# Kernel tuning notes

Measured on AMD Instinct MI355X. Metric: run time of the kernel, lower is better.

The kernel has to match this reference:

```python
import jax, jax.numpy as jnp
import numpy as np

B, N, D_VIS, D_LBL = 64, 256, 2048, 512
H, F_OUT = 8, 256            # n_heads, gat_out_per_head_dim
D_IN = D_VIS + D_LBL         # 2560, GAT input dim
D_GAT = H * F_OUT            # 2048, concat-heads output dim
D_EMB = 512                  # final_embedding_dim
ALPHA = 0.2                  # LeakyReLU negative slope


def setup_inputs() -> dict:
    key = jax.random.key(0)
    ks = jax.random.split(key, 9)
    visual_features = jax.random.normal(ks[0], (B, D_VIS), jnp.float32)
    labels_features = jax.random.normal(ks[1], (N, D_LBL), jnp.float32)
    adj = (jax.random.uniform(ks[2], (N, N)) < 0.1).astype(jnp.float32)
    label_adj_matrix = jnp.maximum(adj, jnp.eye(N, dtype=jnp.float32))
    s = 1.0 / np.sqrt(D_IN)
    W_gat = jax.random.uniform(ks[3], (D_IN, H, F_OUT), jnp.float32, -s, s)
    a_src = jax.random.uniform(ks[4], (H, F_OUT), jnp.float32, -s, s)
    a_dst = jax.random.uniform(ks[5], (H, F_OUT), jnp.float32, -s, s)
    sg = 1.0 / np.sqrt(D_GAT)
    pool_q = jax.random.uniform(ks[6], (D_GAT,), jnp.float32, -sg, sg)
    fc_W = jax.random.uniform(ks[7], (D_GAT, D_EMB), jnp.float32, -sg, sg)
    fc_b = jax.random.uniform(ks[8], (D_EMB,), jnp.float32, -sg, sg)
    return {"visual_features": visual_features, "labels_features": labels_features,
            "label_adj_matrix": label_adj_matrix, "W_gat": W_gat, "a_src": a_src,
            "a_dst": a_dst, "pool_q": pool_q, "fc_W": fc_W, "fc_b": fc_b}


def reference(visual_features, labels_features, label_adj_matrix,
              W_gat, a_src, a_dst, pool_q, fc_W, fc_b):
    # Build per-sample contextualized label node features: (B, N, D_IN)
    x = jnp.concatenate(
        [jnp.broadcast_to(labels_features[None], (B, N, D_LBL)),
         jnp.broadcast_to(visual_features[:, None, :], (B, N, D_VIS))], axis=-1)
    # Multi-head GAT layer, batched over B (the torch code loops over B)
    Wh = jnp.einsum('bnd,dhf->bnhf', x, W_gat)            # (B, N, H, F)
    src = jnp.einsum('bnhf,hf->bhn', Wh, a_src)           # (B, H, N)
    dst = jnp.einsum('bnhf,hf->bhn', Wh, a_dst)           # (B, H, N)
    e = src[:, :, :, None] + dst[:, :, None, :]           # (B, H, N, N)
    e = jnp.where(e > 0, e, ALPHA * e)                    # LeakyReLU
    mask = (label_adj_matrix > 0)[None, None]             # (1, 1, N, N)
    scores = jnp.where(mask, e, jnp.float32(-9e15))
    attn = jax.nn.softmax(scores, axis=-1)                # (B, H, N, N)
    out = jnp.einsum('bhij,bjhf->bihf', attn, Wh)         # (B, N, H, F)
    out = jax.nn.elu(out.reshape(B, N, D_GAT))            # concat heads + ELU
    # attention pooling over label nodes
    pw = jax.nn.softmax(jnp.einsum('bnd,d->bn', out, pool_q), axis=-1)
    pooled = jnp.einsum('bn,bnd->bd', pw, out)            # (B, D_GAT)
    return pooled @ fc_W + fc_b                           # (B, D_EMB)
```

## Files before the change

kernel.cpp:

```cpp
#include <hip/hip_runtime.h>
#include <hip/hip_bf16.h>
#include <math.h>

#define BB 64
#define NN 256
#define D_VIS 2048
#define D_LBL 512
#define HH 8
#define FF 256
#define DG 2048
#define DE 512
#define ALPHA 0.2f
#define PSTRIDE 264

using bf16 = __hip_bfloat16;
using short8 = __attribute__((ext_vector_type(8))) short;
using f32x4  = __attribute__((ext_vector_type(4))) float;
__device__ __forceinline__ float b2f(bf16 x) { return __bfloat162float(x); }
__device__ __forceinline__ unsigned short f2bs(float x) {
    bf16 h = __float2bfloat16(x);
    unsigned short u;
    __builtin_memcpy(&u, &h, 2);
    return u;
}

__global__ void __launch_bounds__(256) k_wh(const float* __restrict__ labels,
                                            const float* __restrict__ visual,
                                            const float* __restrict__ Wg,
                                            unsigned short* __restrict__ WhLbT,
                                            float* __restrict__ WhVz,
                                            const float* __restrict__ aSrc,
                                            const float* __restrict__ aDst,
                                            float* __restrict__ srcLp,
                                            float* __restrict__ dstLp,
                                            float* __restrict__ srcVp,
                                            float* __restrict__ dstVp) {
    __shared__ unsigned short As[32][72];
    __shared__ unsigned short Bs[64][72];
    const int t = threadIdx.x;
    const int w = t >> 6;
    const int lane = t & 63;
    const int l15 = lane & 15, quad = lane >> 4;
    const int n0 = blockIdx.x * 64;
    const int p2 = blockIdx.x & 3;
    const int y = blockIdx.y;
    const bool isL = (y < 8);
    const int q = y - 8;
    const int m0  = isL ? y * 32 : (q & 1) * 32;
    const int z   = isL ? 0 : (q >> 1);
    const int kb0 = z * 512;
    const float* A = isL ? labels : visual;
    const int lda  = isL ? D_LBL : D_VIS;
    const float* Wb = Wg + (isL ? 0 : (size_t)D_LBL * DG);

    f32x4 acc[2];
    acc[0] = (f32x4){0.f, 0.f, 0.f, 0.f};
    acc[1] = (f32x4){0.f, 0.f, 0.f, 0.f};

    for (int kc = 0; kc < 8; ++kc) {
        const int kb = kb0 + kc * 64;
#pragma unroll
        for (int p = 0; p < 2; ++p) {
            const int idx = t + 256 * p;
            const int r = idx >> 4, q4 = idx & 15;
            const float4 v = *(const float4*)(A + (size_t)(m0 + r) * lda + kb + 4 * q4);
            unsigned short s4[4] = {f2bs(v.x), f2bs(v.y), f2bs(v.z), f2bs(v.w)};
            __builtin_memcpy(&As[r][4 * q4], s4, 8);
        }
#pragma unroll
        for (int p = 0; p < 4; ++p) {
            const int kk = (t >> 4) + 16 * p;
            const int c4 = (t & 15) * 4;
            const float4 v = *(const float4*)(Wb + (size_t)(kb + kk) * DG + n0 + c4);
            Bs[c4 + 0][kk] = f2bs(v.x);
            Bs[c4 + 1][kk] = f2bs(v.y);
            Bs[c4 + 2][kk] = f2bs(v.z);
            Bs[c4 + 3][kk] = f2bs(v.w);
        }
        __syncthreads();
#pragma unroll
        for (int ks = 0; ks < 2; ++ks) {
            const short8 bf = *(const short8*)&Bs[w * 16 + l15][ks * 32 + quad * 8];
#pragma unroll
            for (int mi = 0; mi < 2; ++mi) {
                const short8 af = *(const short8*)&As[mi * 16 + l15][ks * 32 + quad * 8];
                acc[mi] = __builtin_amdgcn_mfma_f32_16x16x32_bf16(af, bf, acc[mi], 0, 0, 0);
            }
        }
        __syncthreads();
    }
    const int col = n0 + w * 16 + l15;
    const int h = col >> 8;
    const float as = aSrc[col], ad = aDst[col];
    if (isL) {
#pragma unroll
        for (int mi = 0; mi < 2; ++mi) {
            unsigned short s4[4];
#pragma unroll
            for (int r = 0; r < 4; ++r) s4[r] = f2bs(acc[mi][r]);
            __builtin_memcpy(&WhLbT[(size_t)col * NN + m0 + mi * 16 + quad * 4], s4, 8);
        }
#pragma unroll
        for (int mi = 0; mi < 2; ++mi)
#pragma unroll
            for (int r = 0; r < 4; ++r) {
                float sv = acc[mi][r] * as;
                float dv = acc[mi][r] * ad;
#pragma unroll
                for (int off = 1; off < 16; off <<= 1) {
                    sv += __shfl_xor(sv, off);
                    dv += __shfl_xor(dv, off);
                }
                if (l15 == 0) {
                    const int row = m0 + mi * 16 + quad * 4 + r;
                    srcLp[(p2 * NN + row) * HH + h] = sv;
                    dstLp[(p2 * NN + row) * HH + h] = dv;
                }
            }
    } else {
        float* Wv = WhVz + (size_t)z * BB * DG;
#pragma unroll
        for (int mi = 0; mi < 2; ++mi)
#pragma unroll
            for (int r = 0; r < 4; ++r)
                Wv[(size_t)(m0 + mi * 16 + quad * 4 + r) * DG + col] = acc[mi][r];
        const int pv = p2 * 4 + z;
#pragma unroll
        for (int mi = 0; mi < 2; ++mi)
#pragma unroll
            for (int r = 0; r < 4; ++r) {
                float sv = acc[mi][r] * as;
                float dv = acc[mi][r] * ad;
#pragma unroll
                for (int off = 1; off < 16; off <<= 1) {
                    sv += __shfl_xor(sv, off);
                    dv += __shfl_xor(dv, off);
                }
                if (l15 == 0) {
                    const int row = m0 + mi * 16 + quad * 4 + r;
                    srcVp[(pv * BB + row) * HH + h] = sv;
                    dstVp[(pv * BB + row) * HH + h] = dv;
                }
            }
    }
}

__global__ void __launch_bounds__(512, 4) k_gat(const unsigned short* __restrict__ WhLbT,
                                                const float* __restrict__ WhVz,
                                                const float* __restrict__ srcLp,
                                                const float* __restrict__ dstLp,
                                                const float* __restrict__ srcVp,
                                                const float* __restrict__ dstVp,
                                                const float* __restrict__ adj,
                                                const float* __restrict__ pool_q,
                                                bf16* __restrict__ outb,
                                                float* __restrict__ ps_p) {
    const int bid = blockIdx.x;
    const int it = bid & 3;
    const int h  = (bid >> 2) & 7;
    const int b  = bid >> 5;
    const int i0 = it * 64;
    const int t = threadIdx.x;
    const int w = t >> 6;
    const int lane = t & 63;
    const int l15 = lane & 15, quad = lane >> 4;

    __shared__ __align__(16) unsigned short Pl[64][PSTRIDE];
    __shared__ __align__(16) float dls2[2 * NN];
    __shared__ float slsA[64], slsC[64], slsTE[64], inv[64];
    __shared__ float psl[8][64];

    if (t < NN) {
        float dl = 0.f;
#pragma unroll
        for (int p = 0; p < 4; ++p) dl += dstLp[(p * NN + t) * HH + h];
        dls2[2 * t]     = __expf(dl);
        dls2[2 * t + 1] = __expf(ALPHA * dl);
    }
    if (t < 64) {
        float c = 0.f;
#pragma unroll
        for (int p = 0; p < 16; ++p)
            c += srcVp[(p * BB + b) * HH + h] + dstVp[(p * BB + b) * HH + h];
        float sl = 0.f;
#pragma unroll
        for (int p = 0; p < 4; ++p) sl += srcLp[(p * NN + i0 + t) * HH + h];
        const float u = c + sl;
        slsA[t]  = __expf(u);
        slsC[t]  = __expf(ALPHA * u);
        slsTE[t] = __expf(-u);
    }
    const int n0 = w * 32;
    float wv[2] = {0.f, 0.f};
#pragma unroll
    for (int z = 0; z < 4; ++z)
#pragma unroll
        for (int ni = 0; ni < 2; ++ni)
            wv[ni] += WhVz[(size_t)z * BB * DG + (size_t)b * DG + h * FF + n0 + ni * 16 + l15];
    __syncthreads();

    {
        const int g = lane >> 4, s = lane & 15;
#pragma unroll
        for (int rr = 0; rr < 2; ++rr) {
            const int iloc = w * 8 + rr * 4 + g;
            const int i = i0 + iloc;
            const float Ai = slsA[iloc], Ci = slsC[iloc], TEi = slsTE[iloc];
            float pr[16];
            float sum = 0.f;
#pragma unroll
            for (int jj = 0; jj < 8; ++jj) {
                const int j0 = 2 * s + 32 * jj;
                const float2 av = *(const float2*)(adj + (size_t)i * NN + j0);
                const float4 bd = *(const float4*)&dls2[2 * j0];
                const bool g0 = bd.x > TEi;
                const bool g1 = bd.z > TEi;
                float p0 = (g0 ? Ai : Ci) * (g0 ? bd.x : bd.y);
                float p1 = (g1 ? Ai : Ci) * (g1 ? bd.z : bd.w);
                p0 = av.x > 0.f ? p0 : 0.f;
                p1 = av.y > 0.f ? p1 : 0.f;
                pr[2 * jj] = p0; pr[2 * jj + 1] = p1;
                sum += p0 + p1;
            }
#pragma unroll
            for (int off = 1; off < 16; off <<= 1) sum += __shfl_xor(sum, off);
            if (s == 0) inv[iloc] = 1.0f / sum;
#pragma unroll
            for (int jj = 0; jj < 8; ++jj) {
                const unsigned int pk =
                    ((unsigned int)f2bs(pr[2 * jj + 1]) << 16) | f2bs(pr[2 * jj]);
                *(unsigned int*)&Pl[iloc][2 * s + 32 * jj] = pk;
            }
        }
    }
    __syncthreads();

    f32x4 acc[4][2];
#pragma unroll
    for (int mi = 0; mi < 4; ++mi)
#pragma unroll
        for (int ni = 0; ni < 2; ++ni) acc[mi][ni] = (f32x4){0.f, 0.f, 0.f, 0.f};

    const unsigned short* wb = WhLbT + (size_t)(h * FF + n0 + l15) * NN + quad * 8;
    short8 bc0 = *(const short8*)(wb);
    short8 bc1 = *(const short8*)(wb + (size_t)16 * NN);
#pragma unroll
    for (int kc = 0; kc < 8; ++kc) {
        short8 bn0, bn1;
        if (kc < 7) {
            bn0 = *(const short8*)(wb + (kc + 1) * 32);
            bn1 = *(const short8*)(wb + (size_t)16 * NN + (kc + 1) * 32);
        }
        short8 a[4];
#pragma unroll
        for (int mi = 0; mi < 4; ++mi)
            a[mi] = *(const short8*)&Pl[mi * 16 + l15][kc * 32 + quad * 8];
#pragma unroll
        for (int mi = 0; mi < 4; ++mi)
            acc[mi][0] = __builtin_amdgcn_mfma_f32_16x16x32_bf16(a[mi], bc0, acc[mi][0], 0, 0, 0);
#pragma unroll
        for (int mi = 0; mi < 4; ++mi)
            acc[mi][1] = __builtin_amdgcn_mfma_f32_16x16x32_bf16(a[mi], bc1, acc[mi][1], 0, 0, 0);
        bc0 = bn0; bc1 = bn1;
    }

    const float pqv0 = pool_q[h * FF + n0 + l15];
    const float pqv1 = pool_q[h * FF + n0 + 16 + l15];
#pragma unroll
    for (int mi = 0; mi < 4; ++mi)
#pragma unroll
        for (int r = 0; r < 4; ++r) {
            const int row = mi * 16 + quad * 4 + r;
            const float ivr = inv[row];
            bf16* orow = outb + ((size_t)(b * NN + i0 + row)) * DG + h * FF + n0;
            float x0 = fmaf(acc[mi][0][r], ivr, wv[0]);
            float x1 = fmaf(acc[mi][1][r], ivr, wv[1]);
            x0 = x0 > 0.f ? x0 : (__expf(x0) - 1.0f);
            x1 = x1 > 0.f ? x1 : (__expf(x1) - 1.0f);
            orow[l15]      = __float2bfloat16(x0);
            orow[16 + l15] = __float2bfloat16(x1);
            float dot = fmaf(x0, pqv0, x1 * pqv1);
#pragma unroll
            for (int off = 1; off < 16; off <<= 1) dot += __shfl_xor(dot, off);
            if (l15 == 0) psl[w][row] = dot;
        }
    __syncthreads();
    if (t < 64) {
        float s = 0.f;
#pragma unroll
        for (int ww = 0; ww < 8; ++ww) s += psl[ww][t];
        ps_p[((size_t)h * BB + b) * NN + i0 + t] = s;
    }
}

__global__ void __launch_bounds__(256) k_pool(const bf16* __restrict__ outb,
                                              const float* __restrict__ ps_p,
                                              float* __restrict__ pooled,
                                              const float* __restrict__ fcb,
                                              float* __restrict__ out) {
    const int dt = blockIdx.x;
    const int b  = blockIdx.y;
    const int t  = threadIdx.x;
    if (dt < 2) out[b * DE + dt * 256 + t] = fcb[dt * 256 + t];
    __shared__ float wsm[NN];
    __shared__ float redm[4];
    __shared__ float reds[4];
    float v = 0.f;
#pragma unroll
    for (int s = 0; s < 8; ++s)
        v += ps_p[((size_t)s * BB + b) * NN + t];
    float m = v;
#pragma unroll
    for (int off = 32; off; off >>= 1) m = fmaxf(m, __shfl_xor(m, off));
    if ((t & 63) == 0) redm[t >> 6] = m;
    __syncthreads();
    m = fmaxf(fmaxf(redm[0], redm[1]), fmaxf(redm[2], redm[3]));
    const float e = __expf(v - m);
    float s = e;
#pragma unroll
    for (int off = 32; off; off >>= 1) s += __shfl_xor(s, off);
    if ((t & 63) == 0) reds[t >> 6] = s;
    __syncthreads();
    s = reds[0] + reds[1] + reds[2] + reds[3];
    wsm[t] = e / s;
    __syncthreads();
    const int d = dt * 256 + t;
    float acc = 0.f;
    const bf16* base = outb + (size_t)b * NN * DG + d;
#pragma unroll 8
    for (int n = 0; n < NN; ++n)
        acc = fmaf(wsm[n], b2f(base[(size_t)n * DG]), acc);
    pooled[(size_t)b * DG + d] = acc;
}

__global__ void __launch_bounds__(256) k_mgemm(const float* __restrict__ A, int lda,
                                               const float* __restrict__ W, int ldw,
                                               float* __restrict__ C, int ldc,
                                               int kSlice, int kIters) {
    __shared__ unsigned short As[32][72];
    __shared__ unsigned short Bs[64][72];
    const int t = threadIdx.x;
    const int w = t >> 6;
    const int lane = t & 63;
    const int l15 = lane & 15, quad = lane >> 4;
    const int n0 = blockIdx.x * 64;
    const int m0 = blockIdx.y * 32;
    const int kb0 = blockIdx.z * kSlice;
    f32x4 acc[2];
    acc[0] = (f32x4){0.f, 0.f, 0.f, 0.f};
    acc[1] = (f32x4){0.f, 0.f, 0.f, 0.f};
    for (int kc = 0; kc < kIters; ++kc) {
        const int kb = kb0 + kc * 64;
#pragma unroll
        for (int p = 0; p < 2; ++p) {
            const int idx = t + 256 * p;
            const int r = idx >> 4, q4 = idx & 15;
            const float4 v = *(const float4*)(A + (size_t)(m0 + r) * lda + kb + 4 * q4);
            unsigned short s4[4] = {f2bs(v.x), f2bs(v.y), f2bs(v.z), f2bs(v.w)};
            __builtin_memcpy(&As[r][4 * q4], s4, 8);
        }
#pragma unroll
        for (int p = 0; p < 4; ++p) {
            const int kk = (t >> 4) + 16 * p;
            const int c4 = (t & 15) * 4;
            const float4 v = *(const float4*)(W + (size_t)(kb + kk) * ldw + n0 + c4);
            Bs[c4 + 0][kk] = f2bs(v.x);
            Bs[c4 + 1][kk] = f2bs(v.y);
            Bs[c4 + 2][kk] = f2bs(v.z);
            Bs[c4 + 3][kk] = f2bs(v.w);
        }
        __syncthreads();
#pragma unroll
        for (int ks = 0; ks < 2; ++ks) {
            const short8 bf = *(const short8*)&Bs[w * 16 + l15][ks * 32 + quad * 8];
#pragma unroll
            for (int mi = 0; mi < 2; ++mi) {
                const short8 af = *(const short8*)&As[mi * 16 + l15][ks * 32 + quad * 8];
                acc[mi] = __builtin_amdgcn_mfma_f32_16x16x32_bf16(af, bf, acc[mi], 0, 0, 0);
            }
        }
        __syncthreads();
    }
    const int col = n0 + w * 16 + l15;
#pragma unroll
    for (int mi = 0; mi < 2; ++mi)
#pragma unroll
        for (int r = 0; r < 4; ++r)
            atomicAdd(&C[(size_t)(m0 + mi * 16 + quad * 4 + r) * ldc + col], acc[mi][r]);
}

extern "C" void kernel_launch(void* const* d_in, const int* in_sizes, int n_in,
                              void* d_out, int out_size, void* d_ws, size_t ws_size,
                              hipStream_t stream) {
    (void)in_sizes; (void)n_in; (void)out_size; (void)ws_size;
    const float* visual = (const float*)d_in[0];
    const float* labels = (const float*)d_in[1];
    const float* adj    = (const float*)d_in[2];
    const float* Wg     = (const float*)d_in[3];
    const float* a_src  = (const float*)d_in[4];
    const float* a_dst  = (const float*)d_in[5];
    const float* pool_q = (const float*)d_in[6];
    const float* fcW    = (const float*)d_in[7];
    const float* fcb    = (const float*)d_in[8];
    float* out = (float*)d_out;

    float* ws_f   = (float*)d_ws;
    float* WhVz   = ws_f;
    float* srcLp  = WhVz + 4 * BB * DG;
    float* dstLp  = srcLp + 4 * NN * HH;
    float* srcVp  = dstLp + 4 * NN * HH;
    float* dstVp  = srcVp + 16 * BB * HH;
    float* ps_p   = dstVp + 16 * BB * HH;
    float* pooled = ps_p + 8 * BB * NN;
    bf16*  outb   = (bf16*)(pooled + BB * DG);
    unsigned short* WhLbT = (unsigned short*)(outb + (size_t)BB * NN * DG);

    k_wh<<<dim3(DG / 64, 16), 256, 0, stream>>>(labels, visual, Wg, WhLbT, WhVz,
                                                a_src, a_dst, srcLp, dstLp, srcVp, dstVp);

    k_gat<<<BB * HH * 4, 512, 0, stream>>>(WhLbT, WhVz, srcLp, dstLp, srcVp, dstVp,
                                           adj, pool_q, outb, ps_p);

    k_pool<<<dim3(8, BB), 256, 0, stream>>>(outb, ps_p, pooled, fcb, out);

    k_mgemm<<<dim3(DE / 64, BB / 32, 8), 256, 0, stream>>>(
        pooled, DG, fcW, DE, out, DE, 256, 4);
}
```

Baseline: 189.3 us.

## Process all row tiles per (batch, head) block inside k_gat loop

The GAT attention kernel now launches one block per (batch, head) instead of four, and each block loops over the four 64-row tiles. The per-(b,h) prologue (destination and source exponentials, visual bias terms, WhVz loads) is computed once per block rather than once per tile. The pool-score reduction is also reorganised: a single shuffle step followed by a vectorised sum over a padded shared-memory tile replaces the full 16-lane shuffle tree. The cost is fewer blocks in flight and tiles within a block running one after another with extra barriers, which can reduce latency hiding.

Measured after the change: 190.0 us. About the same (+0.4%).

```diff
diff --git a/kernel.cpp b/kernel.cpp
--- a/kernel.cpp
+++ b/kernel.cpp
@@ -156,10 +156,8 @@
                                                 bf16* __restrict__ outb,
                                                 float* __restrict__ ps_p) {
     const int bid = blockIdx.x;
-    const int it = bid & 3;
-    const int h  = (bid >> 2) & 7;
-    const int b  = bid >> 5;
-    const int i0 = it * 64;
+    const int h = bid & 7;
+    const int b = bid >> 3;
     const int t = threadIdx.x;
     const int w = t >> 6;
     const int lane = t & 63;
@@ -167,24 +165,23 @@
 
     __shared__ __align__(16) unsigned short Pl[64][PSTRIDE];
     __shared__ __align__(16) float dls2[2 * NN];
-    __shared__ float slsA[64], slsC[64], slsTE[64], inv[64];
-    __shared__ float psl[8][64];
+    __shared__ float slsA[NN], slsC[NN], slsTE[NN];
+    __shared__ float inv[64];
+    __shared__ __align__(16) float pd[64][68];
 
     if (t < NN) {
-        float dl = 0.f;
-#pragma unroll
-        for (int p = 0; p < 4; ++p) dl += dstLp[(p * NN + t) * HH + h];
+        float dl = 0.f, sl = 0.f;
+#pragma unroll
+        for (int p = 0; p < 4; ++p) {
+            dl += dstLp[(p * NN + t) * HH + h];
+            sl += srcLp[(p * NN + t) * HH + h];
+        }
         dls2[2 * t]     = __expf(dl);
         dls2[2 * t + 1] = __expf(ALPHA * dl);
-    }
-    if (t < 64) {
         float c = 0.f;
 #pragma unroll
         for (int p = 0; p < 16; ++p)
             c += srcVp[(p * BB + b) * HH + h] + dstVp[(p * BB + b) * HH + h];
-        float sl = 0.f;
-#pragma unroll
-        for (int p = 0; p < 4; ++p) sl += srcLp[(p * NN + i0 + t) * HH + h];
         const float u = c + sl;
         slsA[t]  = __expf(u);
         slsC[t]  = __expf(ALPHA * u);
@@ -197,99 +194,105 @@
 #pragma unroll
         for (int ni = 0; ni < 2; ++ni)
             wv[ni] += WhVz[(size_t)z * BB * DG + (size_t)b * DG + h * FF + n0 + ni * 16 + l15];
-    __syncthreads();
-
-    {
-        const int g = lane >> 4, s = lane & 15;
-#pragma unroll
-        for (int rr = 0; rr < 2; ++rr) {
-            const int iloc = w * 8 + rr * 4 + g;
-            const int i = i0 + iloc;
-            const float Ai = slsA[iloc], Ci = slsC[iloc], TEi = slsTE[iloc];
-            float pr[16];
-            float sum = 0.f;
-#pragma unroll
-            for (int jj = 0; jj < 8; ++jj) {
-                const int j0 = 2 * s + 32 * jj;
-                const float2 av = *(const float2*)(adj + (size_t)i * NN + j0);
-                const float4 bd = *(const float4*)&dls2[2 * j0];
-                const bool g0 = bd.x > TEi;
-                const bool g1 = bd.z > TEi;
-                float p0 = (g0 ? Ai : Ci) * (g0 ? bd.x : bd.y);
-                float p1 = (g1 ? Ai : Ci) * (g1 ? bd.z : bd.w);
-                p0 = av.x > 0.f ? p0 : 0.f;
-                p1 = av.y > 0.f ? p1 : 0.f;
-                pr[2 * jj] = p0; pr[2 * jj + 1] = p1;
-                sum += p0 + p1;
-            }
-#pragma unroll
-            for (int off = 1; off < 16; off <<= 1) sum += __shfl_xor(sum, off);
-            if (s == 0) inv[iloc] = 1.0f / sum;
-#pragma unroll
-            for (int jj = 0; jj < 8; ++jj) {
-                const unsigned int pk =
-                    ((unsigned int)f2bs(pr[2 * jj + 1]) << 16) | f2bs(pr[2 * jj]);
-                *(unsigned int*)&Pl[iloc][2 * s + 32 * jj] = pk;
-            }
-        }
-    }
-    __syncthreads();
-
-    f32x4 acc[4][2];
-#pragma unroll
-    for (int mi = 0; mi < 4; ++mi)
-#pragma unroll
-        for (int ni = 0; ni < 2; ++ni) acc[mi][ni] = (f32x4){0.f, 0.f, 0.f, 0.f};
-
-    const unsigned short* wb = WhLbT + (size_t)(h * FF + n0 + l15) * NN + quad * 8;
-    short8 bc0 = *(const short8*)(wb);
-    short8 bc1 = *(const short8*)(wb + (size_t)16 * NN);
-#pragma unroll
-    for (int kc = 0; kc < 8; ++kc) {
-        short8 bn0, bn1;
-        if (kc < 7) {
-            bn0 = *(const short8*)(wb + (kc + 1) * 32);
-            bn1 = *(const short8*)(wb + (size_t)16 * NN + (kc + 1) * 32);
-        }
-        short8 a[4];
-#pragma unroll
-        for (int mi = 0; mi < 4; ++mi)
-            a[mi] = *(const short8*)&Pl[mi * 16 + l15][kc * 32 + quad * 8];
-#pragma unroll
-        for (int mi = 0; mi < 4; ++mi)
-            acc[mi][0] = __builtin_amdgcn_mfma_f32_16x16x32_bf16(a[mi], bc0, acc[mi][0], 0, 0, 0);
-#pragma unroll
-        for (int mi = 0; mi < 4; ++mi)
-            acc[mi][1] = __builtin_amdgcn_mfma_f32_16x16x32_bf16(a[mi], bc1, acc[mi][1], 0, 0, 0);
-        bc0 = bn0; bc1 = bn1;
-    }
-
     const float pqv0 = pool_q[h * FF + n0 + l15];
     const float pqv1 = pool_q[h * FF + n0 + 16 + l15];
-#pragma unroll
-    for (int mi = 0; mi < 4; ++mi)
-#pragma unroll
-        for (int r = 0; r < 4; ++r) {
-            const int row = mi * 16 + quad * 4 + r;
-            const float ivr = inv[row];
-            bf16* orow = outb + ((size_t)(b * NN + i0 + row)) * DG + h * FF + n0;
-            float x0 = fmaf(acc[mi][0][r], ivr, wv[0]);
-            float x1 = fmaf(acc[mi][1][r], ivr, wv[1]);
-            x0 = x0 > 0.f ? x0 : (__expf(x0) - 1.0f);
-            x1 = x1 > 0.f ? x1 : (__expf(x1) - 1.0f);
-            orow[l15]      = __float2bfloat16(x0);
-            orow[16 + l15] = __float2bfloat16(x1);
-            float dot = fmaf(x0, pqv0, x1 * pqv1);
-#pragma unroll
-            for (int off = 1; off < 16; off <<= 1) dot += __shfl_xor(dot, off);
-            if (l15 == 0) psl[w][row] = dot;
-        }
+    const unsigned short* wb = WhLbT + (size_t)(h * FF + n0 + l15) * NN + quad * 8;
     __syncthreads();
-    if (t < 64) {
-        float s = 0.f;
-#pragma unroll
-        for (int ww = 0; ww < 8; ++ww) s += psl[ww][t];
-        ps_p[((size_t)h * BB + b) * NN + i0 + t] = s;
+
+    for (int it = 0; it < 4; ++it) {
+        const int i0 = it * 64;
+
+        {
+            const int g = lane >> 4, s = lane & 15;
+#pragma unroll
+            for (int rr = 0; rr < 2; ++rr) {
+                const int iloc = w * 8 + rr * 4 + g;
+                const int i = i0 + iloc;
+                const float Ai = slsA[i], Ci = slsC[i], TEi = slsTE[i];
+                float pr[16];
+                float sum = 0.f;
+#pragma unroll
+                for (int jj = 0; jj < 8; ++jj) {
+                    const int j0 = 2 * s + 32 * jj;
+                    const float2 av = *(const float2*)(adj + (size_t)i * NN + j0);
+                    const float4 bd = *(const float4*)&dls2[2 * j0];
+                    const bool g0 = bd.x > TEi;
+                    const bool g1 = bd.z > TEi;
+                    float p0 = (g0 ? Ai : Ci) * (g0 ? bd.x : bd.y);
+                    float p1 = (g1 ? Ai : Ci) * (g1 ? bd.z : bd.w);
+                    p0 = av.x > 0.f ? p0 : 0.f;
+                    p1 = av.y > 0.f ? p1 : 0.f;
+                    pr[2 * jj] = p0; pr[2 * jj + 1] = p1;
+                    sum += p0 + p1;
+                }
+#pragma unroll
+                for (int off = 1; off < 16; off <<= 1) sum += __shfl_xor(sum, off);
+                if (s == 0) inv[iloc] = 1.0f / sum;
+#pragma unroll
+                for (int jj = 0; jj < 8; ++jj) {
+                    const unsigned int pk =
+                        ((unsigned int)f2bs(pr[2 * jj + 1]) << 16) | f2bs(pr[2 * jj]);
+                    *(unsigned int*)&Pl[iloc][2 * s + 32 * jj] = pk;
+                }
+            }
+        }
+        __syncthreads();
+
+        f32x4 acc[4][2];
+#pragma unroll
+        for (int mi = 0; mi < 4; ++mi)
+#pragma unroll
+            for (int ni = 0; ni < 2; ++ni) acc[mi][ni] = (f32x4){0.f, 0.f, 0.f, 0.f};
+
+        short8 bc0 = *(const short8*)(wb);
+        short8 bc1 = *(const short8*)(wb + (size_t)16 * NN);
+#pragma unroll
+        for (int kc = 0; kc < 8; ++kc) {
+            short8 bn0, bn1;
+            if (kc < 7) {
+                bn0 = *(const short8*)(wb + (kc + 1) * 32);
+                bn1 = *(const short8*)(wb + (size_t)16 * NN + (kc + 1) * 32);
+            }
+            short8 a[4];
+#pragma unroll
+            for (int mi = 0; mi < 4; ++mi)
+                a[mi] = *(const short8*)&Pl[mi * 16 + l15][kc * 32 + quad * 8];
+#pragma unroll
+            for (int mi = 0; mi < 4; ++mi)
+                acc[mi][0] = __builtin_amdgcn_mfma_f32_16x16x32_bf16(a[mi], bc0, acc[mi][0], 0, 0, 0);
+#pragma unroll
+            for (int mi = 0; mi < 4; ++mi)
+                acc[mi][1] = __builtin_amdgcn_mfma_f32_16x16x32_bf16(a[mi], bc1, acc[mi][1], 0, 0, 0);
+            bc0 = bn0; bc1 = bn1;
+        }
+
+#pragma unroll
+        for (int mi = 0; mi < 4; ++mi)
+#pragma unroll
+            for (int r = 0; r < 4; ++r) {
+                const int row = mi * 16 + quad * 4 + r;
+                const float ivr = inv[row];
+                bf16* orow = outb + ((size_t)(b * NN + i0 + row)) * DG + h * FF + n0;
+                float x0 = fmaf(acc[mi][0][r], ivr, wv[0]);
+                float x1 = fmaf(acc[mi][1][r], ivr, wv[1]);
+                x0 = x0 > 0.f ? x0 : (__expf(x0) - 1.0f);
+                x1 = x1 > 0.f ? x1 : (__expf(x1) - 1.0f);
+                orow[l15]      = __float2bfloat16(x0);
+                orow[16 + l15] = __float2bfloat16(x1);
+                float dot = fmaf(x0, pqv0, x1 * pqv1);
+                dot += __shfl_xor(dot, 8);
+                if (l15 < 8) pd[row][w * 8 + l15] = dot;
+            }
+        __syncthreads();
+        if (t < 64) {
+            float s4 = 0.f;
+#pragma unroll
+            for (int i = 0; i < 16; ++i) {
+                const f32x4 v = *(const f32x4*)&pd[t][4 * i];
+                s4 += v[0] + v[1] + v[2] + v[3];
+            }
+            ps_p[((size_t)h * BB + b) * NN + i0 + t] = s4;
+        }
     }
 }
 
@@ -418,8 +421,8 @@
     k_wh<<<dim3(DG / 64, 16), 256, 0, stream>>>(labels, visual, Wg, WhLbT, WhVz,
                                                 a_src, a_dst, srcLp, dstLp, srcVp, dstVp);
 
-    k_gat<<<BB * HH * 4, 512, 0, stream>>>(WhLbT, WhVz, srcLp, dstLp, srcVp, dstVp,
-                                           adj, pool_q, outb, ps_p);
+    k_gat<<<BB * HH, 512, 0, stream>>>(WhLbT, WhVz, srcLp, dstLp, srcVp, dstVp,
+                                       adj, pool_q, outb, ps_p);
 
     k_pool<<<dim3(8, BB), 256, 0, stream>>>(outb, ps_p, pooled, fcb, out);
 
```
